# Kernel optimization log

Measured on AMD Instinct MI355X. Metric: run time of the kernel, lower is better.

## Reference

```python
import jax, jax.numpy as jnp
import numpy as np
import math

EMBED = 256
HEADS = 8
HD = EMBED // HEADS  # 32
NB = 3               # n_behaviors
C = NB * NB + 1      # 10 behavior-pair classes
NUM_BUCKETS = 32
MAX_DIST = 40
EPS = 1e-12
B, L = 4, 512


def _rel_bucket(seq_len, num_buckets=NUM_BUCKETS, max_distance=MAX_DIST):
    """T5-style relative position buckets, matching RelativePositionBias._relative_position_bucket."""
    pos = jnp.arange(seq_len)
    relative_position = pos[None, :] - pos[:, None]  # k - q
    n = -relative_position
    nb = num_buckets // 2
    ret = (n < 0).astype(jnp.int32) * nb
    n = jnp.abs(n)
    max_exact = nb // 2
    is_small = n < max_exact
    nf = jnp.maximum(n, 1).astype(jnp.float32)  # clamp to avoid log(0); masked by is_small anyway
    val_large = max_exact + (jnp.log(nf / max_exact) / math.log(max_distance / max_exact) * (nb - max_exact)).astype(jnp.int32)
    val_large = jnp.minimum(val_large, nb - 1)
    return ret + jnp.where(is_small, n, val_large)


def setup_inputs() -> dict:
    key = jax.random.key(0)
    ks = jax.random.split(key, 12)
    s = 0.02
    return {
        "input_tensor": jax.random.normal(ks[0], (B, L, EMBED), jnp.float32),
        "attention_mask": jnp.zeros((B, 1, L, L), jnp.float32),
        "type_seq": jax.random.randint(ks[1], (B, L), 0, NB + 1),
        "Wq": jax.random.normal(ks[2], (NB + 1, EMBED, HEADS, HD), jnp.float32) * s,
        "Wk": jax.random.normal(ks[3], (NB + 1, EMBED, HEADS, HD), jnp.float32) * s,
        "Wv": jax.random.normal(ks[4], (NB + 1, EMBED, HEADS, HD), jnp.float32) * s,
        "W1": jax.random.normal(ks[5], (NB, HEADS, HD, HD), jnp.float32) * s,
        "alpha1": jax.random.normal(ks[6], (C, NB, HEADS), jnp.float32),
        "W2": jax.random.normal(ks[7], (NB, HEADS, HD, HD), jnp.float32) * s,
        "alpha2": jax.random.normal(ks[8], (C, NB, HEADS), jnp.float32),
        "rp_tables": jax.random.normal(ks[9], (C, NUM_BUCKETS, HEADS), jnp.float32) * s,
        "ln_gamma": jnp.ones((EMBED,), jnp.float32),
        "ln_beta": jnp.zeros((EMBED,), jnp.float32),
    }


def reference(input_tensor, attention_mask, type_seq, Wq, Wk, Wv, W1, alpha1, W2, alpha2, rp_tables, ln_gamma, ln_beta):
    bsz, seq_len, emb = input_tensor.shape
    ts = type_seq
    # behavior pair matrix: 0 if either side is padding, else (tq-1)*NB + tk in [1, NB^2]
    bm = ((ts[:, :, None] * ts[:, None, :]) != 0).astype(jnp.int32)
    bm = bm * ((ts[:, :, None] - 1) * NB + ts[:, None, :])  # [B,L,L]

    # --- relative position bias, gathered per behavior pair ---
    bucket = _rel_bucket(seq_len)                 # [L,L]
    vals = rp_tables[:, bucket, :]                # [C,L,L,H]
    qi = jnp.arange(seq_len)[None, :, None]
    ki = jnp.arange(seq_len)[None, None, :]
    bias = vals[bm, qi, ki]                       # [B,L,L,H] gathered along C per pair
    bias = jnp.transpose(bias, (0, 3, 1, 2))      # [B,H,L,L]

    # --- behavior-gated QKV ---
    oh = jax.nn.one_hot(ts, NB + 1, dtype=input_tensor.dtype)  # [B,L,NB+1]
    q = jnp.einsum('BLH,bHhd,BLb->BhLd', input_tensor, Wq, oh)
    k = jnp.einsum('BLH,bHhd,BLb->BhLd', input_tensor, Wk, oh)
    v = jnp.einsum('BLH,bHhd,BLb->BhLd', input_tensor, Wv, oh)

    # --- bilinear scores with per-pair mixing matrices ---
    W1_ = jnp.einsum('bhmn,Cbh->Chmn', W1, jax.nn.softmax(alpha1, axis=1))
    att_all = jnp.einsum('BhQm,Chmn,BhKn->BhQKC', q, W1_, k)  # [B,H,L,L,C]
    scores = jnp.take_along_axis(att_all, bm[:, None, :, :, None], axis=4)[..., 0]
    scores = scores * (1.0 / math.sqrt(HD)) + bias + attention_mask
    probs = jax.nn.softmax(scores, axis=-1)  # dropout=0.0 -> identity

    # --- behavior-mixed value aggregation ---
    W2_ = jnp.einsum('bhmn,Cbh->Chmn', W2, jax.nn.softmax(alpha2, axis=1))
    oh_bm = jax.nn.one_hot(bm, C, dtype=probs.dtype)          # [B,L,L,C]
    pC = probs[:, :, :, :, None] * oh_bm[:, None]             # [B,H,L,L,C]
    ctx = jnp.einsum('BhQKC,Chnm,BhKn->BhQm', pC, W2_, v)     # [B,H,L,d]

    ctx = jnp.transpose(ctx, (0, 2, 1, 3)).reshape(bsz, seq_len, emb)
    x = ctx + input_tensor  # out_dropout=0.0
    mu = jnp.mean(x, axis=-1, keepdims=True)
    var = jnp.mean(jnp.square(x - mu), axis=-1, keepdims=True)
    return (x - mu) / jnp.sqrt(var + EPS) * ln_gamma + ln_beta
```

## Files before the change

### kernel.cpp

```cpp
#include <hip/hip_runtime.h>
#include <math.h>

#define BB 4
#define LL 512
#define EMB 256
#define NH 8
#define HD 32
#define NB_ 3
#define CCN 10
#define NBKT 32
#define SCALE 0.17677669529663687f

typedef __bf16 bf16_t;
typedef __attribute__((ext_vector_type(8))) bf16_t bf16x8;
typedef __attribute__((ext_vector_type(4))) float f32x4;

__device__ __forceinline__ unsigned short f2b(float f) {
    unsigned int u = __float_as_uint(f);
    u += 0x7FFF + ((u >> 16) & 1);
    return (unsigned short)(u >> 16);
}
__device__ __forceinline__ float b2f(unsigned short s) {
    return __uint_as_float(((unsigned int)s) << 16);
}
__device__ __forceinline__ unsigned pack2(float a, float b) {
    return (unsigned)f2b(a) | ((unsigned)f2b(b) << 16);
}
__device__ __forceinline__ int bm_of(int tq, int tk) {
    return (tq * tk != 0) ? ((tq - 1) * 3 + tk) : 0;
}
__device__ __forceinline__ unsigned long long shfl_up64(unsigned long long v, int d) {
    unsigned lo = (unsigned)__shfl_up((int)(unsigned)v, d, 64);
    unsigned hi = (unsigned)__shfl_up((int)(v >> 32), d, 64);
    return (((unsigned long long)hi) << 32) | lo;
}

__device__ __forceinline__ void sort512(const int* __restrict__ tsb, int* spk,
                                        unsigned long long* wtll, int* msc, int tid) {
    int ty0 = tsb[2 * tid], ty1 = tsb[2 * tid + 1];
    unsigned long long pk = (1ULL << (16 * ty0)) + (1ULL << (16 * ty1));
    unsigned long long v = pk;
    int lane = tid & 63;
#pragma unroll
    for (int off = 1; off < 64; off <<= 1) {
        unsigned long long o = shfl_up64(v, off);
        if (lane >= off) v += o;
    }
    int w = tid >> 6;
    if (lane == 63) wtll[w] = v;
    __syncthreads();
    unsigned long long pre = 0, tot = 0;
#pragma unroll
    for (int i = 0; i < 4; i++) {
        unsigned long long xx = wtll[i];
        if (i < w) pre += xx;
        tot += xx;
    }
    v += pre;
    unsigned long long excl = v - pk;
    int c0 = (int)(tot & 0xFFFF), c1 = (int)((tot >> 16) & 0xFFFF);
    int c2 = (int)((tot >> 32) & 0xFFFF), c3 = (int)((tot >> 48) & 0xFFFF);
    int ub0 = 0, ub1 = c0, ub2 = c0 + c1, ub3 = c0 + c1 + c2;
    if (tid == 0) {
        int pc0 = (c0 + 31) & ~31, pc1 = (c1 + 31) & ~31, pc2 = (c2 + 31) & ~31, pc3 = (c3 + 31) & ~31;
        int pb1 = pc0, pb2 = pc0 + pc1, pb3 = pc0 + pc1 + pc2;
        msc[0] = 0;  msc[1] = pb1; msc[2] = pb2; msc[3] = pb3;
        msc[4] = ub0; msc[5] = ub1; msc[6] = ub2; msc[7] = ub3;
        msc[8] = c0; msc[9] = c1; msc[10] = c2; msc[11] = c3;
        msc[12] = (pb3 + pc3 + 63) & ~63;
    }
    int bases[4] = {ub0, ub1, ub2, ub3};
    int r0 = (int)((excl >> (16 * ty0)) & 0xFFFF);
    unsigned long long excl1 = excl + (1ULL << (16 * ty0));
    int r1 = (int)((excl1 >> (16 * ty1)) & 0xFFFF);
    spk[bases[ty0] + r0] = (ty0 << 16) | (2 * tid);
    spk[bases[ty1] + r1] = (ty1 << 16) | (2 * tid + 1);
    __syncthreads();
}

__device__ __forceinline__ void pad_lookup(const int* msc, int pos, int& real, int& upos, int& seg) {
    seg = (pos >= msc[1]) + (pos >= msc[2]) + (pos >= msc[3]);
    int r = pos - msc[seg];
    real = (r < msc[8 + seg]) ? 1 : 0;
    upos = msc[4 + seg] + r;
}

__global__ __launch_bounds__(256, 4) void k_main(
    const float* __restrict__ x, const int* __restrict__ ts,
    const float* __restrict__ Wq, const float* __restrict__ Wk, const float* __restrict__ Wv,
    const float* __restrict__ A1, const float* __restrict__ W1,
    const float* __restrict__ A2, const float* __restrict__ W2,
    const float* __restrict__ am,
    float* __restrict__ W1s, float* __restrict__ W2s,
    unsigned short* __restrict__ W1Tb, unsigned short* __restrict__ W2Tb,
    int* __restrict__ mfl,
    int* __restrict__ spkg, int* __restrict__ mscg, int* __restrict__ kpadg,
    short* __restrict__ tblg,
    unsigned short* __restrict__ qp, unsigned short* __restrict__ kp,
    unsigned short* __restrict__ vpT) {
    __shared__ int spk[LL];
    __shared__ unsigned long long wtll[4];
    __shared__ int msc[16];
    __shared__ __align__(16) unsigned short vt_l[128 * 33];

    int g = blockIdx.x, tid = threadIdx.x;

    if (g >= 384) {
        int gg = g - 384;
        if (gg < 160) {
            float* cmbf = (float*)vt_l;
            int idx = gg;
            const float* alpha = (idx < 80) ? A1 : A2;
            const float* W     = (idx < 80) ? W1 : W2;
            float* Ws          = (idx < 80) ? W1s : W2s;
            unsigned short* WT = (idx < 80) ? W1Tb : W2Tb;
            idx %= 80;
            int cc = idx / NH, h = idx % NH;
            float a0 = alpha[cc * NB_ * NH + 0 * NH + h];
            float a1 = alpha[cc * NB_ * NH + 1 * NH + h];
            float a2 = alpha[cc * NB_ * NH + 2 * NH + h];
            float mx = fmaxf(a0, fmaxf(a1, a2));
            float e0 = __expf(a0 - mx), e1 = __expf(a1 - mx), e2 = __expf(a2 - mx);
            float inv = 1.0f / (e0 + e1 + e2);
            e0 *= inv; e1 *= inv; e2 *= inv;
            for (int i = tid; i < HD * HD; i += 256) {
                int m = i >> 5, n = i & 31;
                float acc = e0 * W[((0 * NH + h) * HD + m) * HD + n]
                          + e1 * W[((1 * NH + h) * HD + m) * HD + n]
                          + e2 * W[((2 * NH + h) * HD + m) * HD + n];
                cmbf[m * 33 + n] = acc;
            }
            __syncthreads();
            for (int i = tid; i < HD * HD; i += 256) {
                int a = i >> 5, bq = i & 31;
                Ws[((cc * NH + h) * HD + a) * HD + bq] = cmbf[a * 33 + bq];
                WT[((size_t)(cc * NH + h) * HD + a) * HD + bq] = f2b(cmbf[bq * 33 + a]);
            }
            return;
        }
        if (gg < 288) {
            int* reds = (int*)wtll;
            int idx = gg - 160;
            const uint4* p = (const uint4*)am + (size_t)idx * 2048;
            unsigned o = 0;
#pragma unroll
            for (int j = 0; j < 8; j++) {
                uint4 v = p[tid + j * 256];
                o |= v.x | v.y | v.z | v.w;
            }
            int wv = __any(o != 0);
            if ((tid & 63) == 0) reds[tid >> 6] = wv;
            __syncthreads();
            if (tid == 0) mfl[idx] = reds[0] | reds[1] | reds[2] | reds[3];
            return;
        }
        if (gg < 292) {
            int b = gg - 288;
            sort512(ts + b * LL, spk, wtll, msc, tid);
            for (int i = tid; i < LL; i += 256) spkg[b * LL + i] = spk[i];
            if (tid < 16) mscg[b * 16 + tid] = msc[tid];
            int KT = msc[12];
            for (int pos = tid; pos < KT; pos += 256) {
                int real, upos, seg;
                pad_lookup(msc, pos, real, upos, seg);
                int orig = real ? (spk[upos] & 0xFFFF) : 0x3FF;
                kpadg[b * 640 + pos] = (seg << 20) | ((real ? upos : 0) << 10) | orig;
            }
            return;
        }
        for (int d = tid; d < LL; d += 256) {
            int v;
            if (d < 8) v = d;
            else {
                double r = log((double)d / 8.0) / log(5.0);
                v = 8 + (int)(r * 8.0);
                if (v > 15) v = 15;
            }
            tblg[d] = (short)v;
        }
        return;
    }

    int ns = g % 6, gb = g / 6;
    int b = gb >> 4, tb = gb & 15, i0 = tb * 32;
    int which = ns >> 1, nh = ns & 1;
    int wave = tid >> 6, lane = tid & 63, quad = lane >> 4, col = lane & 15;

    sort512(ts + b * LL, spk, wtll, msc, tid);

    bf16x8 afr[2][8];
#pragma unroll
    for (int mt = 0; mt < 2; mt++) {
        int orig = spk[i0 + mt * 16 + col] & 0xFFFF;
        const float* xr = &x[(size_t)(b * LL + orig) * EMB];
#pragma unroll
        for (int kc = 0; kc < 8; kc++) {
            float4 v0 = *(const float4*)&xr[kc * 32 + quad * 8];
            float4 v1 = *(const float4*)&xr[kc * 32 + quad * 8 + 4];
            uint4 up;
            up.x = pack2(v0.x, v0.y); up.y = pack2(v0.z, v0.w);
            up.z = pack2(v1.x, v1.y); up.w = pack2(v1.z, v1.w);
            afr[mt][kc] = *(bf16x8*)&up;
        }
    }
    int t_start = spk[i0] >> 16, t_end = spk[i0 + 31] >> 16;
    unsigned short* outp = (which == 0) ? qp : kp;
    const float* wmat = (which == 0) ? Wq : (which == 1) ? Wk : Wv;

    int n_0 = nh * 128 + (wave * 2 + 0) * 16 + col;

    for (int ty = t_start; ty <= t_end; ty++) {
        const float* wty = wmat + (size_t)ty * EMB * EMB;
        const float* wc0 = wty + (size_t)(quad * 8) * EMB + n_0;
        const float* wc1 = wc0 + 16;
        f32x4 acc[2][2];
#pragma unroll
        for (int mt = 0; mt < 2; mt++)
#pragma unroll
            for (int nt = 0; nt < 2; nt++) acc[mt][nt] = (f32x4){0.f, 0.f, 0.f, 0.f};
#pragma unroll
        for (int kc = 0; kc < 8; kc++) {
            const float* p0 = wc0 + (size_t)kc * 32 * EMB;
            const float* p1 = wc1 + (size_t)kc * 32 * EMB;
            float f0[8], f1[8];
#pragma unroll
            for (int j = 0; j < 8; j++) { f0[j] = p0[j * EMB]; f1[j] = p1[j * EMB]; }
            uint4 u0, u1;
            u0.x = pack2(f0[0], f0[1]); u0.y = pack2(f0[2], f0[3]);
            u0.z = pack2(f0[4], f0[5]); u0.w = pack2(f0[6], f0[7]);
            u1.x = pack2(f1[0], f1[1]); u1.y = pack2(f1[2], f1[3]);
            u1.z = pack2(f1[4], f1[5]); u1.w = pack2(f1[6], f1[7]);
            bf16x8 b0 = *(bf16x8*)&u0;
            bf16x8 b1 = *(bf16x8*)&u1;
            acc[0][0] = __builtin_amdgcn_mfma_f32_16x16x32_bf16(afr[0][kc], b0, acc[0][0], 0, 0, 0);
            acc[0][1] = __builtin_amdgcn_mfma_f32_16x16x32_bf16(afr[0][kc], b1, acc[0][1], 0, 0, 0);
            acc[1][0] = __builtin_amdgcn_mfma_f32_16x16x32_bf16(afr[1][kc], b0, acc[1][0], 0, 0, 0);
            acc[1][1] = __builtin_amdgcn_mfma_f32_16x16x32_bf16(afr[1][kc], b1, acc[1][1], 0, 0, 0);
        }
        if (which < 2) {
#pragma unroll
            for (int mt = 0; mt < 2; mt++)
#pragma unroll
                for (int r = 0; r < 4; r++) {
                    int tokloc = mt * 16 + quad * 4 + r;
                    int tty = spk[i0 + tokloc] >> 16;
                    if (tty != ty) continue;
#pragma unroll
                    for (int nt = 0; nt < 2; nt++) {
                        int n = n_0 + nt * 16;
                        int h = n >> 5, d = n & 31;
                        outp[((size_t)(b * NH + h) * LL + i0 + tokloc) * HD + d] = f2b(acc[mt][nt][r]);
                    }
                }
        } else {
#pragma unroll
            for (int mt = 0; mt < 2; mt++)
#pragma unroll
                for (int nt = 0; nt < 2; nt++) {
                    int ln = (wave * 2 + nt) * 16 + col;
#pragma unroll
                    for (int r = 0; r < 4; r++)
                        vt_l[ln * 33 + mt * 16 + quad * 4 + r] = f2b(acc[mt][nt][r]);
                }
            __syncthreads();
            int ub = msc[4 + ty], cnt = msc[8 + ty], pb = msc[ty];
            int lo = ub - i0; if (lo < 0) lo = 0;
            int hi = ub + cnt - i0; if (hi > 32) hi = 32;
            int run = hi - lo;
            int pbase = pb + i0 + lo - ub;
            int rowbase = b * 256 + nh * 128;
            int t32 = tid & 31;
            if (t32 < run) {
                for (int rr = tid >> 5; rr < 128; rr += 8)
                    vpT[(size_t)(rowbase + rr) * 640 + pbase + t32] = vt_l[rr * 33 + lo + t32];
            }
            __syncthreads();
        }
    }
}

#define SCP 648
#define OFF_UN   20736
#define OFF_QTB  29184
#define OFF_KPAD 33536
#define OFF_TBL  36096
#define OFF_RPL  37120
#define OFF_QOR  38400
#define OFF_QTY  38464
#define OFF_INV  38528
#define OFF_PSUM 38592
#define SM_TOTAL 38848
__global__ __launch_bounds__(256, 4) void k_attn(
    const unsigned short* __restrict__ qp, const unsigned short* __restrict__ kp,
    const unsigned short* __restrict__ vpT,
    const int* __restrict__ spkg, const int* __restrict__ mscg, const int* __restrict__ kpadg,
    const short* __restrict__ tblg,
    const float* __restrict__ rp, const float* __restrict__ am,
    const float* __restrict__ W1s, const float* __restrict__ W2s,
    const unsigned short* __restrict__ W1Tb, const unsigned short* __restrict__ W2Tb,
    const int* __restrict__ mfl, float* __restrict__ ctx) {
    __shared__ __align__(16) char smem[SM_TOTAL];
    __shared__ int msk_s;
    unsigned short* scu = (unsigned short*)smem;
    unsigned short* qstb = (unsigned short*)(smem + OFF_UN);
    float* sb   = (float*)(smem + OFF_UN);
    unsigned short* qtb = (unsigned short*)(smem + OFF_QTB);
    unsigned short* sbb = (unsigned short*)(smem + OFF_QTB);
    int*   kpad = (int*)(smem + OFF_KPAD);
    short* tbl  = (short*)(smem + OFF_TBL);
    float* rp_l = (float*)(smem + OFF_RPL);
    int*   qor_l = (int*)(smem + OFF_QOR);
    int*   qty_l = (int*)(smem + OFF_QTY);
    float* inv_l = (float*)(smem + OFF_INV);
    float* psum = (float*)(smem + OFF_PSUM);

    int blk = blockIdx.x;
    int b = blk >> 8, h = (blk >> 5) & 7, q16 = blk & 31;
    int i0q = q16 * 16;
    int tid = threadIdx.x;
    int wave = tid >> 6, lane = tid & 63, quad = lane >> 4, col = lane & 15;
    int bh = b * NH + h;

    int KT = mscg[b * 16 + 12];
    if (wave == 0) {
        int v = mfl[lane] | mfl[64 + lane];
        int anyv = __any(v != 0);
        if (lane == 0) msk_s = anyv;
    }
    if (tid < 16) {
        int v = spkg[b * LL + i0q + tid];
        qor_l[tid] = v & 0xFFFF; qty_l[tid] = v >> 16;
    }
    if (tid < (KT >> 2)) ((int4*)kpad)[tid] = ((const int4*)(kpadg + b * 640))[tid];
    ((int*)tbl)[tid] = ((const int*)tblg)[tid];
    for (int i = tid; i < CCN * NBKT; i += 256) rp_l[i] = rp[i * NH + h];
    {
        int q = tid >> 4, m2 = (tid & 15) * 2;
        ((unsigned*)qstb)[q * 20 + (tid & 15)] =
            *(const unsigned*)&qp[((size_t)bh * LL + i0q + q) * HD + m2];
    }
    __syncthreads();

    int qor_r[4], qty_r[4];
#pragma unroll
    for (int r = 0; r < 4; r++) { qor_r[r] = qor_l[quad * 4 + r]; qty_r[r] = qty_l[quad * 4 + r]; }
    bool uniq = (qty_l[0] == qty_l[15]);
    int tqu = qty_l[0];
    int tA = qty_l[0], tB = qty_l[15];
    bool two = false;
    if (!uniq) {
        two = true;
#pragma unroll
        for (int i = 0; i < 16; i++) {
            int t = qty_l[i];
            two = two && (t == tA || t == tB);
        }
    }
    int mz = (msk_s == 0);

    if (uniq) {
#pragma unroll
        for (int it = 0; it < 2; it++) {
            int t8 = wave * 2 + it;
            int tk = t8 >> 1, nhf = t8 & 1;
            int bmv = bm_of(tqu, tk);
            bf16x8 a = *(const bf16x8*)&qstb[col * 40 + quad * 8];
            bf16x8 bb = *(const bf16x8*)&W1Tb[((size_t)(bmv * NH + h) * HD + nhf * 16 + col) * HD + quad * 8];
            f32x4 d = {0.f, 0.f, 0.f, 0.f};
            d = __builtin_amdgcn_mfma_f32_16x16x32_bf16(a, bb, d, 0, 0, 0);
#pragma unroll
            for (int r = 0; r < 4; r++)
                qtb[(quad * 4 + r) * 136 + tk * 32 + nhf * 16 + col] = f2b(d[r]);
        }
    } else if (two) {
#pragma unroll
        for (int it = 0; it < 2; it++) {
            int t8 = wave * 2 + it;
            int tk = t8 >> 1, nhf = t8 & 1;
            bf16x8 a = *(const bf16x8*)&qstb[col * 40 + quad * 8];
            bf16x8 bA = *(const bf16x8*)&W1Tb[((size_t)(bm_of(tA, tk) * NH + h) * HD + nhf * 16 + col) * HD + quad * 8];
            bf16x8 bBv = *(const bf16x8*)&W1Tb[((size_t)(bm_of(tB, tk) * NH + h) * HD + nhf * 16 + col) * HD + quad * 8];
            f32x4 dA = {0.f, 0.f, 0.f, 0.f};
            f32x4 dB = {0.f, 0.f, 0.f, 0.f};
            dA = __builtin_amdgcn_mfma_f32_16x16x32_bf16(a, bA, dA, 0, 0, 0);
            dB = __builtin_amdgcn_mfma_f32_16x16x32_bf16(a, bBv, dB, 0, 0, 0);
#pragma unroll
            for (int r = 0; r < 4; r++) {
                float val = (qty_r[r] == tA) ? dA[r] : dB[r];
                qtb[(quad * 4 + r) * 136 + tk * 32 + nhf * 16 + col] = f2b(val);
            }
        }
    } else {
        for (int i = tid; i < 16 * 128; i += 256) {
            int q = i >> 7, r = i & 127, tk = r >> 5, n = r & 31;
            int bmv = bm_of(qty_l[q], tk);
            const float* wb = &W1s[((bmv * NH + h) * HD) * HD + n];
            float acc = 0.f;
#pragma unroll
            for (int m = 0; m < HD; m++) acc += b2f(qstb[q * 40 + m]) * wb[m * HD];
            qtb[q * 136 + tk * 32 + n] = f2b(acc);
        }
    }
    __syncthreads();

    const float* amb = am + (size_t)b * LL * LL;
    int ntiles = KT >> 4;
    if (mz) {
        float rs[4] = {0.f, 0.f, 0.f, 0.f};
        int tqm_r[4], tqz_r[4];
#pragma unroll
        for (int r = 0; r < 4; r++) { tqm_r[r] = (qty_r[r] - 1) * 3; tqz_r[r] = (qty_r[r] != 0); }
        for (int tile = wave; tile < ntiles; tile += 4) {
            int kb = tile * 16;
            int kv0 = kpad[kb];
            if ((kv0 & 0x3FF) == 0x3FF) {
#pragma unroll
                for (int r = 0; r < 4; r++) scu[(quad * 4 + r) * SCP + kb + col] = 0;
                continue;
            }
            int tkt = kv0 >> 20;
            int kpi = kb + col;
            int kv = kpad[kpi];
            int ko = kv & 0x3FF;
            int upos = (kv >> 10) & 0x3FF;
            bool real = (ko != 0x3FF);
            bf16x8 bfr;
            if (real) bfr = *(const bf16x8*)&kp[((size_t)bh * LL + upos) * HD + quad * 8];
            else { uint4 z = make_uint4(0, 0, 0, 0); bfr = *(bf16x8*)&z; }
            bf16x8 a = *(const bf16x8*)&qtb[col * 136 + tkt * 32 + quad * 8];
            f32x4 d = {0.f, 0.f, 0.f, 0.f};
            d = __builtin_amdgcn_mfma_f32_16x16x32_bf16(a, bfr, d, 0, 0, 0);
            if (!real) {
#pragma unroll
                for (int r = 0; r < 4; r++) scu[(quad * 4 + r) * SCP + kpi] = 0;
            } else {
#pragma unroll
                for (int r = 0; r < 4; r++) {
                    int q = quad * 4 + r;
                    int qo = qor_r[r];
                    int dd = qo - ko;
                    int ad = dd < 0 ? -dd : dd;
                    int bk = (dd < 0 ? 16 : 0) + (int)tbl[ad];
                    int bmv = (tqz_r[r] && tkt) ? tqm_r[r] + tkt : 0;
                    float sv = d[r] * SCALE + rp_l[bmv * NBKT + bk];
                    float e = __expf(sv);
                    scu[q * SCP + kpi] = f2b(e);
                    rs[r] += e;
                }
            }
        }
#pragma unroll
        for (int off = 1; off < 16; off <<= 1) {
#pragma unroll
            for (int r = 0; r < 4; r++) rs[r] += __shfl_xor(rs[r], off, 16);
        }
        if (col == 0) {
#pragma unroll
            for (int r = 0; r < 4; r++) psum[wave * 16 + quad * 4 + r] = rs[r];
        }
    } else {
        for (int tile = wave; tile < ntiles; tile += 4) {
            int kb = tile * 16;
            int kv0 = kpad[kb];
            if ((kv0 & 0x3FF) == 0x3FF) {
#pragma unroll
                for (int r = 0; r < 4; r++) scu[(quad * 4 + r) * SCP + kb + col] = 0xFF80;
                continue;
            }
            int tkt = kv0 >> 20;
            int kpi = kb + col;
            int kv = kpad[kpi];
            int ko = kv & 0x3FF;
            int upos = (kv >> 10) & 0x3FF;
            bool real = (ko != 0x3FF);
            bf16x8 bfr;
            if (real) bfr = *(const bf16x8*)&kp[((size_t)bh * LL + upos) * HD + quad * 8];
            else { uint4 z = make_uint4(0, 0, 0, 0); bfr = *(bf16x8*)&z; }
            bf16x8 a = *(const bf16x8*)&qtb[col * 136 + tkt * 32 + quad * 8];
            f32x4 d = {0.f, 0.f, 0.f, 0.f};
            d = __builtin_amdgcn_mfma_f32_16x16x32_bf16(a, bfr, d, 0, 0, 0);
            if (!real) {
#pragma unroll
                for (int r = 0; r < 4; r++) scu[(quad * 4 + r) * SCP + kpi] = 0xFF80;
            } else {
#pragma unroll
                for (int r = 0; r < 4; r++) {
                    int q = quad * 4 + r;
                    int qo = qor_r[r];
                    int dd = qo - ko;
                    int ad = dd < 0 ? -dd : dd;
                    int bk = (dd < 0 ? 16 : 0) + (int)tbl[ad];
                    float sv = d[r] * SCALE + rp_l[bm_of(qty_r[r], tkt) * NBKT + bk];
                    sv += amb[(size_t)qo * LL + ko];
                    scu[q * SCP + kpi] = f2b(sv);
                }
            }
        }
    }
    __syncthreads();

    if (mz) {
        if (tid < 16)
            inv_l[tid] = 1.0f / (psum[tid] + psum[16 + tid] + psum[32 + tid] + psum[48 + tid]);
    } else {
        int gq = tid >> 4, t16 = tid & 15;
        float mx = -1e30f;
        for (int kk = t16; kk < KT; kk += 16) mx = fmaxf(mx, b2f(scu[gq * SCP + kk]));
#pragma unroll
        for (int off = 1; off < 16; off <<= 1) mx = fmaxf(mx, __shfl_xor(mx, off, 16));
        float sum = 0.f;
        for (int kk = t16; kk < KT; kk += 16) {
            int idx = gq * SCP + kk;
            float e = __expf(b2f(scu[idx]) - mx);
            scu[idx] = f2b(e); sum += e;
        }
#pragma unroll
        for (int off = 1; off < 16; off <<= 1) sum += __shfl_xor(sum, off, 16);
        if (t16 == 0) inv_l[gq] = 1.0f / sum;
    }
    __syncthreads();

    const unsigned short* vbase = &vpT[(size_t)(b * 256 + h * 32) * 640];
    f32x4 accv[2];
    accv[0] = (f32x4){0.f, 0.f, 0.f, 0.f};
    accv[1] = (f32x4){0.f, 0.f, 0.f, 0.f};
    {
        int pb = mscg[b * 16 + wave];
        int cnt = mscg[b * 16 + 8 + wave];
        int g0 = pb >> 5, g1 = (pb + cnt + 31) >> 5;
        for (int gg = g0; gg < g1; ++gg) {
            int loc = gg << 5;
            bf16x8 a = *(const bf16x8*)&scu[col * SCP + loc + quad * 8];
            bf16x8 b0 = *(const bf16x8*)&vbase[(size_t)col * 640 + loc + quad * 8];
            bf16x8 b1 = *(const bf16x8*)&vbase[(size_t)(col + 16) * 640 + loc + quad * 8];
            accv[0] = __builtin_amdgcn_mfma_f32_16x16x32_bf16(a, b0, accv[0], 0, 0, 0);
            accv[1] = __builtin_amdgcn_mfma_f32_16x16x32_bf16(a, b1, accv[1], 0, 0, 0);
        }
    }
#pragma unroll
    for (int hh = 0; hh < 2; hh++)
#pragma unroll
        for (int r = 0; r < 4; r++) {
            int q = quad * 4 + r, n = col + 16 * hh;
            float fin = accv[hh][r];
            sb[q * 132 + wave * 32 + n] = fin;
            sbb[q * 136 + wave * 32 + n] = f2b(fin);
        }
    __syncthreads();

    if (uniq) {
        if (wave < 2) {
            int mhf = wave;
            f32x4 d = {0.f, 0.f, 0.f, 0.f};
#pragma unroll
            for (int tk = 0; tk < 4; tk++) {
                int bmv = bm_of(tqu, tk);
                bf16x8 a = *(const bf16x8*)&sbb[col * 136 + tk * 32 + quad * 8];
                bf16x8 bb = *(const bf16x8*)&W2Tb[((size_t)(bmv * NH + h) * HD + mhf * 16 + col) * HD + quad * 8];
                d = __builtin_amdgcn_mfma_f32_16x16x32_bf16(a, bb, d, 0, 0, 0);
            }
#pragma unroll
            for (int r = 0; r < 4; r++) {
                int q = quad * 4 + r;
                ctx[((size_t)(b * LL + qor_l[q])) * EMB + h * HD + mhf * 16 + col] = d[r] * inv_l[q];
            }
        }
    } else if (two) {
        int myT = (wave < 2) ? tA : tB;
        int mhf = wave & 1;
        f32x4 d = {0.f, 0.f, 0.f, 0.f};
#pragma unroll
        for (int tk = 0; tk < 4; tk++) {
            int bmv = bm_of(myT, tk);
            bf16x8 a = *(const bf16x8*)&sbb[col * 136 + tk * 32 + quad * 8];
            bf16x8 bb = *(const bf16x8*)&W2Tb[((size_t)(bmv * NH + h) * HD + mhf * 16 + col) * HD + quad * 8];
            d = __builtin_amdgcn_mfma_f32_16x16x32_bf16(a, bb, d, 0, 0, 0);
        }
#pragma unroll
        for (int r = 0; r < 4; r++) {
            int q = quad * 4 + r;
            if (qty_l[q] == myT)
                ctx[((size_t)(b * LL + qor_l[q])) * EMB + h * HD + mhf * 16 + col] = d[r] * inv_l[q];
        }
    } else {
        int m = tid & 31, qq = tid >> 5;
#pragma unroll
        for (int rep = 0; rep < 2; rep++) {
            int qi = qq + 8 * rep;
            int tq = qty_l[qi];
            float acc = 0.f;
#pragma unroll
            for (int tk2 = 0; tk2 < 4; tk2++) {
                int bmv = bm_of(tq, tk2);
                const float* wb = &W2s[((bmv * NH + h) * HD) * HD + m];
                const float* sbp = &sb[qi * 132 + tk2 * 32];
                for (int n = 0; n < HD; n++) acc += sbp[n] * wb[n * HD];
            }
            int qo = qor_l[qi];
            ctx[((size_t)(b * LL + qo)) * EMB + h * HD + m] = acc * inv_l[qi];
        }
    }
}

__global__ void k_ln(const float* __restrict__ ctx, const float* __restrict__ x,
                     const float* __restrict__ gamma, const float* __restrict__ beta,
                     float* __restrict__ out) {
    int wave = threadIdx.x >> 6, lane = threadIdx.x & 63;
    int tok = blockIdx.x * 4 + wave;
    size_t base = (size_t)tok * EMB + lane * 4;
    float4 c = *(const float4*)&ctx[base];
    float4 xi = *(const float4*)&x[base];
    float4 v;
    v.x = c.x + xi.x; v.y = c.y + xi.y; v.z = c.z + xi.z; v.w = c.w + xi.w;
    float s = v.x + v.y + v.z + v.w;
    float s2 = v.x * v.x + v.y * v.y + v.z * v.z + v.w * v.w;
#pragma unroll
    for (int off = 1; off < 64; off <<= 1) {
        s += __shfl_xor(s, off, 64);
        s2 += __shfl_xor(s2, off, 64);
    }
    float mu = s * (1.0f / EMB);
    float var = s2 * (1.0f / EMB) - mu * mu;
    float r = rsqrtf(var + 1e-12f);
    float4 gg = *(const float4*)&gamma[lane * 4];
    float4 bb = *(const float4*)&beta[lane * 4];
    float4 o;
    o.x = (v.x - mu) * r * gg.x + bb.x;
    o.y = (v.y - mu) * r * gg.y + bb.y;
    o.z = (v.z - mu) * r * gg.z + bb.z;
    o.w = (v.w - mu) * r * gg.w + bb.w;
    *(float4*)&out[base] = o;
}

extern "C" void kernel_launch(void* const* d_in, const int* in_sizes, int n_in,
                              void* d_out, int out_size, void* d_ws, size_t ws_size,
                              hipStream_t stream) {
    const float* x  = (const float*)d_in[0];
    const float* am = (const float*)d_in[1];
    const int*   ts = (const int*)d_in[2];
    const float* Wq = (const float*)d_in[3];
    const float* Wk = (const float*)d_in[4];
    const float* Wv = (const float*)d_in[5];
    const float* W1 = (const float*)d_in[6];
    const float* a1 = (const float*)d_in[7];
    const float* W2 = (const float*)d_in[8];
    const float* a2 = (const float*)d_in[9];
    const float* rp = (const float*)d_in[10];
    const float* g  = (const float*)d_in[11];
    const float* be = (const float*)d_in[12];
    float* out = (float*)d_out;

    float* ws  = (float*)d_ws;
    float* W1s = ws;
    float* W2s = ws + 81920;
    unsigned short* W1Tb = (unsigned short*)(ws + 163840);
    unsigned short* W2Tb = (unsigned short*)(ws + 204800);
    int* mfl  = (int*)(ws + 245760);
    int* spkg = (int*)(ws + 246016);
    int* mscg = (int*)(ws + 248064);
    int* kpadg = (int*)(ws + 248128);
    short* tblg = (short*)(ws + 250688);
    unsigned short* qp = (unsigned short*)(ws + 250944);
    unsigned short* kp = qp + BB * NH * LL * HD;
    unsigned short* vpT = kp + BB * NH * LL * HD;
    float* ctx = (float*)(vpT + BB * 256 * 640);

    hipLaunchKernelGGL(k_main, dim3(677), dim3(256), 0, stream,
                       x, ts, Wq, Wk, Wv, a1, W1, a2, W2, am,
                       W1s, W2s, W1Tb, W2Tb, mfl, spkg, mscg, kpadg, tblg,
                       qp, kp, vpT);
    hipLaunchKernelGGL(k_attn, dim3(BB * NH * 32), dim3(256), 0, stream,
                       qp, kp, vpT, spkg, mscg, kpadg, tblg, rp, am, W1s, W2s, W1Tb, W2Tb,
                       mfl, ctx);
    hipLaunchKernelGGL(k_ln, dim3(BB * LL / 4), dim3(256), 0, stream, ctx, x, g, be, out);
}
```

Baseline: 118.9 us.

## Double attention block to 512 threads and split key tiles across eight waves

The attention kernel now launches 512 threads (eight waves) per block instead of 256. The score and exp loop strides key tiles by eight waves, and the P·V accumulation gives each segment to two waves that handle alternating 32-key groups. The two partial sums are combined through shared memory with an extra barrier. Row sums are reduced over eight partials. This aims to expose more parallelism per query tile at the cost of a larger block, more synchronisation and some idle waves in the serial sections.

Measured after the change: 116.9 us (median of 2 runs). About the same (-1.7%).

```diff
diff --git a/kernel.cpp b/kernel.cpp
--- a/kernel.cpp
+++ b/kernel.cpp
@@ -289,8 +289,8 @@
 #define OFF_QTY  38464
 #define OFF_INV  38528
 #define OFF_PSUM 38592
-#define SM_TOTAL 38848
-__global__ __launch_bounds__(256, 4) void k_attn(
+#define SM_TOTAL 39104
+__global__ __launch_bounds__(512, 8) void k_attn(
     const unsigned short* __restrict__ qp, const unsigned short* __restrict__ kp,
     const unsigned short* __restrict__ vpT,
     const int* __restrict__ spkg, const int* __restrict__ mscg, const int* __restrict__ kpadg,
@@ -332,9 +332,9 @@
         qor_l[tid] = v & 0xFFFF; qty_l[tid] = v >> 16;
     }
     if (tid < (KT >> 2)) ((int4*)kpad)[tid] = ((const int4*)(kpadg + b * 640))[tid];
-    ((int*)tbl)[tid] = ((const int*)tblg)[tid];
-    for (int i = tid; i < CCN * NBKT; i += 256) rp_l[i] = rp[i * NH + h];
-    {
+    if (tid < 256) ((int*)tbl)[tid] = ((const int*)tblg)[tid];
+    for (int i = tid; i < CCN * NBKT; i += 512) rp_l[i] = rp[i * NH + h];
+    if (tid < 256) {
         int q = tid >> 4, m2 = (tid & 15) * 2;
         ((unsigned*)qstb)[q * 20 + (tid & 15)] =
             *(const unsigned*)&qp[((size_t)bh * LL + i0q + q) * HD + m2];
@@ -359,39 +359,31 @@
     int mz = (msk_s == 0);
 
     if (uniq) {
-#pragma unroll
-        for (int it = 0; it < 2; it++) {
-            int t8 = wave * 2 + it;
-            int tk = t8 >> 1, nhf = t8 & 1;
-            int bmv = bm_of(tqu, tk);
-            bf16x8 a = *(const bf16x8*)&qstb[col * 40 + quad * 8];
-            bf16x8 bb = *(const bf16x8*)&W1Tb[((size_t)(bmv * NH + h) * HD + nhf * 16 + col) * HD + quad * 8];
-            f32x4 d = {0.f, 0.f, 0.f, 0.f};
-            d = __builtin_amdgcn_mfma_f32_16x16x32_bf16(a, bb, d, 0, 0, 0);
-#pragma unroll
-            for (int r = 0; r < 4; r++)
-                qtb[(quad * 4 + r) * 136 + tk * 32 + nhf * 16 + col] = f2b(d[r]);
-        }
+        int tk = wave >> 1, nhf = wave & 1;
+        int bmv = bm_of(tqu, tk);
+        bf16x8 a = *(const bf16x8*)&qstb[col * 40 + quad * 8];
+        bf16x8 bb = *(const bf16x8*)&W1Tb[((size_t)(bmv * NH + h) * HD + nhf * 16 + col) * HD + quad * 8];
+        f32x4 d = {0.f, 0.f, 0.f, 0.f};
+        d = __builtin_amdgcn_mfma_f32_16x16x32_bf16(a, bb, d, 0, 0, 0);
+#pragma unroll
+        for (int r = 0; r < 4; r++)
+            qtb[(quad * 4 + r) * 136 + tk * 32 + nhf * 16 + col] = f2b(d[r]);
     } else if (two) {
-#pragma unroll
-        for (int it = 0; it < 2; it++) {
-            int t8 = wave * 2 + it;
-            int tk = t8 >> 1, nhf = t8 & 1;
-            bf16x8 a = *(const bf16x8*)&qstb[col * 40 + quad * 8];
-            bf16x8 bA = *(const bf16x8*)&W1Tb[((size_t)(bm_of(tA, tk) * NH + h) * HD + nhf * 16 + col) * HD + quad * 8];
-            bf16x8 bBv = *(const bf16x8*)&W1Tb[((size_t)(bm_of(tB, tk) * NH + h) * HD + nhf * 16 + col) * HD + quad * 8];
-            f32x4 dA = {0.f, 0.f, 0.f, 0.f};
-            f32x4 dB = {0.f, 0.f, 0.f, 0.f};
-            dA = __builtin_amdgcn_mfma_f32_16x16x32_bf16(a, bA, dA, 0, 0, 0);
-            dB = __builtin_amdgcn_mfma_f32_16x16x32_bf16(a, bBv, dB, 0, 0, 0);
-#pragma unroll
-            for (int r = 0; r < 4; r++) {
-                float val = (qty_r[r] == tA) ? dA[r] : dB[r];
-                qtb[(quad * 4 + r) * 136 + tk * 32 + nhf * 16 + col] = f2b(val);
-            }
+        int tk = wave >> 1, nhf = wave & 1;
+        bf16x8 a = *(const bf16x8*)&qstb[col * 40 + quad * 8];
+        bf16x8 bA = *(const bf16x8*)&W1Tb[((size_t)(bm_of(tA, tk) * NH + h) * HD + nhf * 16 + col) * HD + quad * 8];
+        bf16x8 bBv = *(const bf16x8*)&W1Tb[((size_t)(bm_of(tB, tk) * NH + h) * HD + nhf * 16 + col) * HD + quad * 8];
+        f32x4 dA = {0.f, 0.f, 0.f, 0.f};
+        f32x4 dB = {0.f, 0.f, 0.f, 0.f};
+        dA = __builtin_amdgcn_mfma_f32_16x16x32_bf16(a, bA, dA, 0, 0, 0);
+        dB = __builtin_amdgcn_mfma_f32_16x16x32_bf16(a, bBv, dB, 0, 0, 0);
+#pragma unroll
+        for (int r = 0; r < 4; r++) {
+            float val = (qty_r[r] == tA) ? dA[r] : dB[r];
+            qtb[(quad * 4 + r) * 136 + tk * 32 + nhf * 16 + col] = f2b(val);
         }
     } else {
-        for (int i = tid; i < 16 * 128; i += 256) {
+        for (int i = tid; i < 16 * 128; i += 512) {
             int q = i >> 7, r = i & 127, tk = r >> 5, n = r & 31;
             int bmv = bm_of(qty_l[q], tk);
             const float* wb = &W1s[((bmv * NH + h) * HD) * HD + n];
@@ -410,7 +402,7 @@
         int tqm_r[4], tqz_r[4];
 #pragma unroll
         for (int r = 0; r < 4; r++) { tqm_r[r] = (qty_r[r] - 1) * 3; tqz_r[r] = (qty_r[r] != 0); }
-        for (int tile = wave; tile < ntiles; tile += 4) {
+        for (int tile = wave; tile < ntiles; tile += 8) {
             int kb = tile * 16;
             int kv0 = kpad[kb];
             if ((kv0 & 0x3FF) == 0x3FF) {
@@ -459,7 +451,7 @@
             for (int r = 0; r < 4; r++) psum[wave * 16 + quad * 4 + r] = rs[r];
         }
     } else {
-        for (int tile = wave; tile < ntiles; tile += 4) {
+        for (int tile = wave; tile < ntiles; tile += 8) {
             int kb = tile * 16;
             int kv0 = kpad[kb];
             if ((kv0 & 0x3FF) == 0x3FF) {
@@ -500,9 +492,13 @@
     __syncthreads();
 
     if (mz) {
-        if (tid < 16)
-            inv_l[tid] = 1.0f / (psum[tid] + psum[16 + tid] + psum[32 + tid] + psum[48 + tid]);
-    } else {
+        if (tid < 16) {
+            float s = 0.f;
+#pragma unroll
+            for (int w = 0; w < 8; w++) s += psum[w * 16 + tid];
+            inv_l[tid] = 1.0f / s;
+        }
+    } else if (tid < 256) {
         int gq = tid >> 4, t16 = tid & 15;
         float mx = -1e30f;
         for (int kk = t16; kk < KT; kk += 16) mx = fmaxf(mx, b2f(scu[gq * SCP + kk]));
@@ -525,10 +521,11 @@
     accv[0] = (f32x4){0.f, 0.f, 0.f, 0.f};
     accv[1] = (f32x4){0.f, 0.f, 0.f, 0.f};
     {
-        int pb = mscg[b * 16 + wave];
-        int cnt = mscg[b * 16 + 8 + wave];
+        int seg = wave & 3, halfp = wave >> 2;
+        int pb = mscg[b * 16 + seg];
+        int cnt = mscg[b * 16 + 8 + seg];
         int g0 = pb >> 5, g1 = (pb + cnt + 31) >> 5;
-        for (int gg = g0; gg < g1; ++gg) {
+        for (int gg = g0 + halfp; gg < g1; gg += 2) {
             int loc = gg << 5;
             bf16x8 a = *(const bf16x8*)&scu[col * SCP + loc + quad * 8];
             bf16x8 b0 = *(const bf16x8*)&vbase[(size_t)col * 640 + loc + quad * 8];
@@ -537,15 +534,28 @@
             accv[1] = __builtin_amdgcn_mfma_f32_16x16x32_bf16(a, b1, accv[1], 0, 0, 0);
         }
     }
-#pragma unroll
-    for (int hh = 0; hh < 2; hh++)
-#pragma unroll
-        for (int r = 0; r < 4; r++) {
-            int q = quad * 4 + r, n = col + 16 * hh;
-            float fin = accv[hh][r];
-            sb[q * 132 + wave * 32 + n] = fin;
-            sbb[q * 136 + wave * 32 + n] = f2b(fin);
-        }
+    if (wave < 4) {
+#pragma unroll
+        for (int hh = 0; hh < 2; hh++)
+#pragma unroll
+            for (int r = 0; r < 4; r++) {
+                int q = quad * 4 + r, n = col + 16 * hh;
+                sb[q * 132 + wave * 32 + n] = accv[hh][r];
+            }
+    }
+    __syncthreads();
+    if (wave >= 4) {
+        int seg = wave - 4;
+#pragma unroll
+        for (int hh = 0; hh < 2; hh++)
+#pragma unroll
+            for (int r = 0; r < 4; r++) {
+                int q = quad * 4 + r, n = col + 16 * hh;
+                float fin = sb[q * 132 + seg * 32 + n] + accv[hh][r];
+                sb[q * 132 + seg * 32 + n] = fin;
+                sbb[q * 136 + seg * 32 + n] = f2b(fin);
+            }
+    }
     __syncthreads();
 
     if (uniq) {
@@ -566,23 +576,25 @@
             }
         }
     } else if (two) {
-        int myT = (wave < 2) ? tA : tB;
-        int mhf = wave & 1;
-        f32x4 d = {0.f, 0.f, 0.f, 0.f};
-#pragma unroll
-        for (int tk = 0; tk < 4; tk++) {
-            int bmv = bm_of(myT, tk);
-            bf16x8 a = *(const bf16x8*)&sbb[col * 136 + tk * 32 + quad * 8];
-            bf16x8 bb = *(const bf16x8*)&W2Tb[((size_t)(bmv * NH + h) * HD + mhf * 16 + col) * HD + quad * 8];
-            d = __builtin_amdgcn_mfma_f32_16x16x32_bf16(a, bb, d, 0, 0, 0);
-        }
-#pragma unroll
-        for (int r = 0; r < 4; r++) {
-            int q = quad * 4 + r;
-            if (qty_l[q] == myT)
-                ctx[((size_t)(b * LL + qor_l[q])) * EMB + h * HD + mhf * 16 + col] = d[r] * inv_l[q];
-        }
-    } else {
+        if (wave < 4) {
+            int myT = (wave < 2) ? tA : tB;
+            int mhf = wave & 1;
+            f32x4 d = {0.f, 0.f, 0.f, 0.f};
+#pragma unroll
+            for (int tk = 0; tk < 4; tk++) {
+                int bmv = bm_of(myT, tk);
+                bf16x8 a = *(const bf16x8*)&sbb[col * 136 + tk * 32 + quad * 8];
+                bf16x8 bb = *(const bf16x8*)&W2Tb[((size_t)(bmv * NH + h) * HD + mhf * 16 + col) * HD + quad * 8];
+                d = __builtin_amdgcn_mfma_f32_16x16x32_bf16(a, bb, d, 0, 0, 0);
+            }
+#pragma unroll
+            for (int r = 0; r < 4; r++) {
+                int q = quad * 4 + r;
+                if (qty_l[q] == myT)
+                    ctx[((size_t)(b * LL + qor_l[q])) * EMB + h * HD + mhf * 16 + col] = d[r] * inv_l[q];
+            }
+        }
+    } else if (tid < 256) {
         int m = tid & 31, qq = tid >> 5;
 #pragma unroll
         for (int rep = 0; rep < 2; rep++) {
@@ -669,7 +681,7 @@
                        x, ts, Wq, Wk, Wv, a1, W1, a2, W2, am,
                        W1s, W2s, W1Tb, W2Tb, mfl, spkg, mscg, kpadg, tblg,
                        qp, kp, vpT);
-    hipLaunchKernelGGL(k_attn, dim3(BB * NH * 32), dim3(256), 0, stream,
+    hipLaunchKernelGGL(k_attn, dim3(BB * NH * 32), dim3(512), 0, stream,
                        qp, kp, vpT, spkg, mscg, kpadg, tblg, rp, am, W1s, W2s, W1Tb, W2Tb,
                        mfl, ctx);
     hipLaunchKernelGGL(k_ln, dim3(BB * LL / 4), dim3(256), 0, stream, ctx, x, g, be, out);
```
